# Optimization experiments

Measured on AMD Instinct MI355X. Metric: run time of the kernel, lower is better.

Reference implementation:

```python
import jax, jax.numpy as jnp
import numpy as np

NU = 3
NUM_MEM_TOKENS = 128
EPS = 1e-5


def dpfp(x, nu=NU):
    # x: [..., d] -> [..., 2*nu*d]; all outputs are >= 0
    x = jnp.concatenate([jax.nn.relu(x), jax.nn.relu(-x)], axis=-1)
    x_rolled = jnp.concatenate([jnp.roll(x, shift=j, axis=-1) for j in range(1, nu + 1)], axis=-1)
    x_repeat = jnp.concatenate([x] * nu, axis=-1)
    return x_repeat * x_rolled


def setup_inputs() -> dict:
    key = jax.random.key(0)
    ks = jax.random.split(key, 8)
    B, S, D, DM = 1, 16384, 2048, 64
    DK = 2 * NU * DM  # 384
    scale = 0.02
    return {
        "hidden_states": jax.random.normal(ks[0], (B, S, D), jnp.float32),
        "Wmq": jax.random.normal(ks[1], (DM, D), jnp.float32) * scale,
        "Wmk": jax.random.normal(ks[2], (DM, D), jnp.float32) * scale,
        "Wmv": jax.random.normal(ks[3], (D, D), jnp.float32) * scale,
        "Wmb_w": jax.random.normal(ks[4], (1, D), jnp.float32) * scale,
        "Wmb_b": jax.random.normal(ks[5], (1,), jnp.float32),
        "W_mem": jax.random.normal(ks[6], (B, DK, D), jnp.float32) * scale,
        "z": jax.random.uniform(ks[7], (B, DK), jnp.float32) + 0.1,
    }


def reference(hidden_states, Wmq, Wmk, Wmv, Wmb_w, Wmb_b, W_mem, z):
    # ---- associate (read from fast-weight memory) ----
    mq = dpfp(hidden_states @ Wmq.T)                       # [b,s,dk]
    num = jnp.einsum('ijk,ikt->ijt', mq, W_mem)            # [b,s,d]
    denom = jnp.einsum('ik,ijk->ij', z, mq)[..., None] + EPS
    hidden_states = num / denom + hidden_states

    # wrapped transformer layer modeled as identity
    out = hidden_states

    # ---- update_mem (write: recurrent outer-product accumulation) ----
    mem_tokens = out[:, -NUM_MEM_TOKENS:]                  # [b,m,d]
    mk = dpfp(mem_tokens @ Wmk.T)                          # [b,m,dk]
    new_mv = mem_tokens @ Wmv.T                            # [b,m,d]

    num2 = jnp.einsum('ijk,ikt->ijt', mk, W_mem)           # [b,m,d]
    denom2 = jnp.einsum('ij,ikj->ik', z, mk)[..., None] + EPS
    prev_mv = num2 / denom2

    mk_sq = jnp.sum(mk * mk, axis=-1)                      # ||mk||^2, [b,m]
    new_info_coef = 1.0 - denom2 / (mk_sq + EPS)[..., None]
    new_info_coef = jax.lax.stop_gradient(jnp.clip(new_info_coef, 0.0, 1.0))

    mv = new_mv - prev_mv
    mb = jax.nn.sigmoid(mem_tokens @ Wmb_w.T + Wmb_b)[..., 0]  # [b,m]
    associations = jnp.einsum('ijk,ijt,ij->ikt', mk, mv, mb)   # [b,dk,d]

    W_mem_new = W_mem + associations
    z_new = z + jnp.sum(new_info_coef * mk, axis=1)
    return out, W_mem_new, z_new
```

## Files before the change

kernel.cpp:

```cpp
#include <hip/hip_runtime.h>
#include <hip/hip_bf16.h>
#include <math.h>

#define S_ 16384
#define D_ 2048
#define DM_ 64
#define DK_ 384
#define NMEM_ 128
#define EPS_ 1e-5f

typedef __attribute__((ext_vector_type(8))) short bf16x8;
typedef __attribute__((ext_vector_type(4))) float f32x4;
typedef unsigned short u16;

static __device__ __forceinline__ u16 f2bf(float x) {
    __hip_bfloat16 h = __float2bfloat16(x);
    return *reinterpret_cast<u16*>(&h);
}

static __device__ __forceinline__ void gload16(const void* g, void* l) {
    __builtin_amdgcn_global_load_lds(
        (const __attribute__((address_space(1))) unsigned int*)g,
        (__attribute__((address_space(3))) unsigned int*)l, 16, 0, 0);
}

__global__ __launch_bounds__(256) void k_prep(const float* __restrict__ Wmq,
                                              const float* __restrict__ Wmv,
                                              const float* __restrict__ Wmem,
                                              u16* __restrict__ Wmq_b,
                                              u16* __restrict__ Wmv_b,
                                              u16* __restrict__ WmT) {
    __shared__ float ts[32][33];
    const int bid = blockIdx.x;
    const int tid = threadIdx.x;
    if (bid < 4096) {
        size_t idx = ((size_t)bid * 256 + tid) * 4;
        float4 v = *reinterpret_cast<const float4*>(&Wmv[idx]);
        ushort4 p;
        p.x = f2bf(v.x); p.y = f2bf(v.y); p.z = f2bf(v.z); p.w = f2bf(v.w);
        *reinterpret_cast<ushort4*>(&Wmv_b[idx]) = p;
    } else if (bid < 4224) {
        int idx = ((bid - 4096) * 256 + tid) * 4;
        float4 v = *reinterpret_cast<const float4*>(&Wmq[idx]);
        ushort4 p;
        p.x = f2bf(v.x); p.y = f2bf(v.y); p.z = f2bf(v.z); p.w = f2bf(v.w);
        *reinterpret_cast<ushort4*>(&Wmq_b[idx]) = p;
    } else {
        int t = bid - 4224;
        int c0 = (t & 63) * 32, k0 = (t >> 6) * 32;
        const int tx = tid & 31, ty = tid >> 5;
#pragma unroll
        for (int i = 0; i < 4; ++i)
            ts[ty + 8 * i][tx] = Wmem[(size_t)(k0 + ty + 8 * i) * D_ + c0 + tx];
        __syncthreads();
#pragma unroll
        for (int i = 0; i < 4; ++i)
            WmT[(size_t)(c0 + ty + 8 * i) * DK_ + k0 + tx] = f2bf(ts[tx][ty + 8 * i]);
    }
}

__global__ __launch_bounds__(256) void k_qdp(const float* __restrict__ hs,
                                             const u16* __restrict__ Wmq_b,
                                             const float* __restrict__ z,
                                             u16* __restrict__ mq_b,
                                             float* __restrict__ denomv) {
    __shared__ u16 As[32 * 64];
    __shared__ u16 Bs[64 * 64];
    __shared__ float xs[32][128];
    __shared__ float zs[DK_];
    const int r0 = blockIdx.x * 32;
    const int tid = threadIdx.x;
    const int lane = tid & 63, w = tid >> 6;
    const int lrow = lane & 15, lkg = lane >> 4;
    const int wr = w >> 1, wc = w & 1;
    for (int i = tid; i < DK_; i += 256) zs[i] = z[i];
    f32x4 acc[2];
    const f32x4 zero4 = {0.f, 0.f, 0.f, 0.f};
    acc[0] = zero4; acc[1] = zero4;
    for (int kc = 0; kc < D_ / 64; ++kc) {
#pragma unroll
        for (int i = 0; i < 2; ++i) {
            int flat4 = tid + 256 * i;
            int row = flat4 >> 4, c4 = flat4 & 15;
            const float4 v = *reinterpret_cast<const float4*>(
                &hs[(size_t)(r0 + row) * D_ + kc * 64 + c4 * 4]);
            int off = row * 64 + (((c4 >> 1) ^ (row & 7)) * 8) + (c4 & 1) * 4;
            ushort4 p;
            p.x = f2bf(v.x); p.y = f2bf(v.y); p.z = f2bf(v.z); p.w = f2bf(v.w);
            *reinterpret_cast<ushort4*>(&As[off]) = p;
        }
#pragma unroll
        for (int i = 0; i < 2; ++i) {
            int col = w * 16 + i * 8 + (lane >> 3);
            int gg = (lane & 7) ^ (col & 7);
            gload16(Wmq_b + (size_t)col * D_ + kc * 64 + gg * 8,
                    &Bs[(w * 16 + i * 8) * 64]);
        }
        __syncthreads();
#pragma unroll
        for (int s = 0; s < 2; ++s) {
            int rl = wr * 16 + lrow;
            bf16x8 a_ = *reinterpret_cast<const bf16x8*>(
                &As[rl * 64 + (((s * 4 + lkg) ^ (rl & 7)) * 8)]);
#pragma unroll
            for (int n = 0; n < 2; ++n) {
                int cl = wc * 32 + n * 16 + lrow;
                bf16x8 b_ = *reinterpret_cast<const bf16x8*>(
                    &Bs[cl * 64 + (((s * 4 + lkg) ^ (cl & 7)) * 8)]);
                acc[n] = __builtin_amdgcn_mfma_f32_16x16x32_bf16(a_, b_, acc[n], 0, 0, 0);
            }
        }
        __syncthreads();
    }
#pragma unroll
    for (int n = 0; n < 2; ++n) {
        int col = wc * 32 + n * 16 + lrow;
#pragma unroll
        for (int r = 0; r < 4; ++r) {
            int row = wr * 16 + lkg * 4 + r;
            float q = acc[n][r];
            xs[row][col] = fmaxf(q, 0.f);
            xs[row][col + 64] = fmaxf(-q, 0.f);
        }
    }
    __syncthreads();
    {
        int row = tid >> 3, sub = tid & 7;
        float pd = 0.f;
#pragma unroll
        for (int t = 0; t < 48; ++t) {
            int m = sub * 48 + t;
            int g = m >> 7, i = m & 127;
            float v = xs[row][i] * xs[row][(i - g - 1) & 127];
            mq_b[(size_t)(r0 + row) * DK_ + m] = f2bf(v);
            pd += zs[m] * v;
        }
        pd += __shfl_down(pd, 4, 8);
        pd += __shfl_down(pd, 2, 8);
        pd += __shfl_down(pd, 1, 8);
        if (sub == 0) denomv[r0 + row] = pd + EPS_;
    }
}

__global__ __launch_bounds__(256) void k_main(const float* __restrict__ hs,
                                              const u16* __restrict__ mq_b,
                                              const u16* __restrict__ WmT,
                                              const float* __restrict__ denomv,
                                              float* __restrict__ out) {
    __shared__ u16 At[128 * 128];
    __shared__ u16 Bt[128 * 128];
    __shared__ float dinv[128];
    const int bid = blockIdx.x;
    const int swz = (bid & 7) * 256 + (bid >> 3);
    const int r0 = (swz >> 4) * 128, c0 = (swz & 15) * 128;
    const int tid = threadIdx.x;
    const int lane = tid & 63, w = tid >> 6;
    const int lrow = lane & 15, lkg = lane >> 4;
    const int wr = w >> 1, wc = w & 1;
    if (tid < 128) dinv[tid] = 1.f / denomv[r0 + tid];
    f32x4 acc[4][4];
    const f32x4 zero4 = {0.f, 0.f, 0.f, 0.f};
#pragma unroll
    for (int m = 0; m < 4; ++m)
#pragma unroll
        for (int n = 0; n < 4; ++n) acc[m][n] = zero4;
    for (int kc = 0; kc < 3; ++kc) {
#pragma unroll
        for (int i = 0; i < 8; ++i) {
            int rr = w * 32 + i * 4 + (lane >> 4);
            int gg = (lane & 15) ^ (rr & 7);
            gload16(mq_b + (size_t)(r0 + rr) * DK_ + kc * 128 + gg * 8,
                    &At[(w * 32 + i * 4) * 128]);
            gload16(WmT + (size_t)(c0 + rr) * DK_ + kc * 128 + gg * 8,
                    &Bt[(w * 32 + i * 4) * 128]);
        }
        __syncthreads();
#pragma unroll
        for (int s = 0; s < 4; ++s) {
            bf16x8 af[4], bb[4];
#pragma unroll
            for (int m = 0; m < 4; ++m) {
                int rl = wr * 64 + m * 16 + lrow;
                af[m] = *reinterpret_cast<const bf16x8*>(
                    &At[rl * 128 + (((s * 4 + lkg) ^ (rl & 7)) * 8)]);
            }
#pragma unroll
            for (int n = 0; n < 4; ++n) {
                int cl = wc * 64 + n * 16 + lrow;
                bb[n] = *reinterpret_cast<const bf16x8*>(
                    &Bt[cl * 128 + (((s * 4 + lkg) ^ (cl & 7)) * 8)]);
            }
#pragma unroll
            for (int m = 0; m < 4; ++m)
#pragma unroll
                for (int n = 0; n < 4; ++n)
                    acc[m][n] = __builtin_amdgcn_mfma_f32_16x16x32_bf16(
                        af[m], bb[n], acc[m][n], 0, 0, 0);
        }
        __syncthreads();
    }
#pragma unroll
    for (int m = 0; m < 4; ++m)
#pragma unroll
        for (int n = 0; n < 4; ++n) {
            int colg = c0 + wc * 64 + n * 16 + lrow;
#pragma unroll
            for (int r = 0; r < 4; ++r) {
                int rowl = wr * 64 + m * 16 + lkg * 4 + r;
                size_t off = (size_t)(r0 + rowl) * D_ + colg;
                out[off] = acc[m][n][r] * dinv[rowl] + hs[off];
            }
        }
}

__global__ __launch_bounds__(256) void k_mk(const float* __restrict__ out,
                                            const float* __restrict__ Wmk,
                                            const float* __restrict__ Wmb_w,
                                            const float* __restrict__ Wmb_b,
                                            const float* __restrict__ z,
                                            float* __restrict__ mk_g,
                                            u16* __restrict__ mk_b,
                                            u16* __restrict__ mem_b,
                                            float* __restrict__ scal) {
    __shared__ float memRow[D_];
    __shared__ float qpart[4][64];
    __shared__ float xv[128];
    __shared__ float mks[DK_];
    __shared__ float red[256];
    const int j = blockIdx.x;
    const int tid = threadIdx.x;
    const float* mem = out + (size_t)(S_ - NMEM_ + j) * D_;
    for (int i = tid; i < D_; i += 256) {
        float v = mem[i];
        memRow[i] = v;
        mem_b[(size_t)j * D_ + i] = f2bf(v);
    }
    __syncthreads();
    {
        int c = tid & 63, seg = tid >> 6;
        float p = 0.f;
        for (int k = seg * 512; k < seg * 512 + 512; ++k)
            p += memRow[k] * Wmk[(size_t)c * D_ + k];
        qpart[seg][c] = p;
    }
    __syncthreads();
    if (tid < 64) {
        float q = qpart[0][tid] + qpart[1][tid] + qpart[2][tid] + qpart[3][tid];
        xv[tid] = fmaxf(q, 0.f);
        xv[tid + 64] = fmaxf(-q, 0.f);
    }
    __syncthreads();
    for (int m = tid; m < DK_; m += 256) {
        int i = m & 127, g = m >> 7;
        float v = xv[i] * xv[(i - g - 1) & 127];
        mks[m] = v;
        mk_g[(size_t)j * DK_ + m] = v;
        mk_b[(size_t)j * DK_ + m] = f2bf(v);
    }
    __syncthreads();
    float pd = 0.f, ps = 0.f;
    for (int m = tid; m < DK_; m += 256) { float v = mks[m]; pd += v * z[m]; ps += v * v; }
    red[tid] = pd; __syncthreads();
    for (int s = 128; s > 0; s >>= 1) { if (tid < s) red[tid] += red[tid + s]; __syncthreads(); }
    float denom2 = red[0] + EPS_;
    __syncthreads();
    red[tid] = ps; __syncthreads();
    for (int s = 128; s > 0; s >>= 1) { if (tid < s) red[tid] += red[tid + s]; __syncthreads(); }
    float mksq = red[0];
    __syncthreads();
    float pb = 0.f;
    for (int k = tid; k < D_; k += 256) pb += memRow[k] * Wmb_w[k];
    red[tid] = pb; __syncthreads();
    for (int s = 128; s > 0; s >>= 1) { if (tid < s) red[tid] += red[tid + s]; __syncthreads(); }
    if (tid == 0) {
        float bsum = red[0] + Wmb_b[0];
        float mb = 1.f / (1.f + expf(-bsum));
        float nic = 1.f - denom2 / (mksq + EPS_);
        nic = fminf(fmaxf(nic, 0.f), 1.f);
        scal[j * 4 + 0] = denom2;
        scal[j * 4 + 1] = nic;
        scal[j * 4 + 2] = mb;
        scal[j * 4 + 3] = mksq;
    }
}

__global__ __launch_bounds__(256) void k_mv(const u16* __restrict__ mem_b,
                                            const u16* __restrict__ Wmv_b,
                                            const u16* __restrict__ mk_b,
                                            const u16* __restrict__ WmT,
                                            const float* __restrict__ scal,
                                            float* __restrict__ mvb) {
    __shared__ u16 At[128 * 64];
    __shared__ u16 Bt[64 * 64];
    __shared__ float inv2[128];
    __shared__ float mbl[128];
    const int c0 = blockIdx.x * 64;
    const int tid = threadIdx.x;
    const int lane = tid & 63, w = tid >> 6;
    const int lrow = lane & 15, lkg = lane >> 4;
    const int wr = w >> 1, wc = w & 1;
    if (tid < 128) {
        inv2[tid] = 1.f / scal[tid * 4 + 0];
        mbl[tid] = scal[tid * 4 + 2];
    }
    f32x4 acc1[4][2], acc2[4][2];
    const f32x4 zero4 = {0.f, 0.f, 0.f, 0.f};
#pragma unroll
    for (int m = 0; m < 4; ++m)
#pragma unroll
        for (int n = 0; n < 2; ++n) { acc1[m][n] = zero4; acc2[m][n] = zero4; }
    for (int kc = 0; kc < D_ / 64; ++kc) {
#pragma unroll
        for (int i = 0; i < 4; ++i) {
            int rr = w * 32 + i * 8 + (lane >> 3);
            int gg = (lane & 7) ^ (rr & 7);
            gload16(mem_b + (size_t)rr * D_ + kc * 64 + gg * 8,
                    &At[(w * 32 + i * 8) * 64]);
        }
#pragma unroll
        for (int i = 0; i < 2; ++i) {
            int cc = w * 16 + i * 8 + (lane >> 3);
            int gg = (lane & 7) ^ (cc & 7);
            gload16(Wmv_b + (size_t)(c0 + cc) * D_ + kc * 64 + gg * 8,
                    &Bt[(w * 16 + i * 8) * 64]);
        }
        __syncthreads();
#pragma unroll
        for (int s = 0; s < 2; ++s) {
            bf16x8 af[4], bb[2];
#pragma unroll
            for (int m = 0; m < 4; ++m) {
                int rl = wr * 64 + m * 16 + lrow;
                af[m] = *reinterpret_cast<const bf16x8*>(
                    &At[rl * 64 + (((s * 4 + lkg) ^ (rl & 7)) * 8)]);
            }
#pragma unroll
            for (int n = 0; n < 2; ++n) {
                int cl = wc * 32 + n * 16 + lrow;
                bb[n] = *reinterpret_cast<const bf16x8*>(
                    &Bt[cl * 64 + (((s * 4 + lkg) ^ (cl & 7)) * 8)]);
            }
#pragma unroll
            for (int m = 0; m < 4; ++m)
#pragma unroll
                for (int n = 0; n < 2; ++n)
                    acc1[m][n] = __builtin_amdgcn_mfma_f32_16x16x32_bf16(
                        af[m], bb[n], acc1[m][n], 0, 0, 0);
        }
        __syncthreads();
    }
    for (int kc = 0; kc < 6; ++kc) {
#pragma unroll
        for (int i = 0; i < 4; ++i) {
            int rr = w * 32 + i * 8 + (lane >> 3);
            int gg = (lane & 7) ^ (rr & 7);
            gload16(mk_b + (size_t)rr * DK_ + kc * 64 + gg * 8,
                    &At[(w * 32 + i * 8) * 64]);
        }
#pragma unroll
        for (int i = 0; i < 2; ++i) {
            int cc = w * 16 + i * 8 + (lane >> 3);
            int gg = (lane & 7) ^ (cc & 7);
            gload16(WmT + (size_t)(c0 + cc) * DK_ + kc * 64 + gg * 8,
                    &Bt[(w * 16 + i * 8) * 64]);
        }
        __syncthreads();
#pragma unroll
        for (int s = 0; s < 2; ++s) {
            bf16x8 af[4], bb[2];
#pragma unroll
            for (int m = 0; m < 4; ++m) {
                int rl = wr * 64 + m * 16 + lrow;
                af[m] = *reinterpret_cast<const bf16x8*>(
                    &At[rl * 64 + (((s * 4 + lkg) ^ (rl & 7)) * 8)]);
            }
#pragma unroll
            for (int n = 0; n < 2; ++n) {
                int cl = wc * 32 + n * 16 + lrow;
                bb[n] = *reinterpret_cast<const bf16x8*>(
                    &Bt[cl * 64 + (((s * 4 + lkg) ^ (cl & 7)) * 8)]);
            }
#pragma unroll
            for (int m = 0; m < 4; ++m)
#pragma unroll
                for (int n = 0; n < 2; ++n)
                    acc2[m][n] = __builtin_amdgcn_mfma_f32_16x16x32_bf16(
                        af[m], bb[n], acc2[m][n], 0, 0, 0);
        }
        __syncthreads();
    }
#pragma unroll
    for (int m = 0; m < 4; ++m)
#pragma unroll
        for (int n = 0; n < 2; ++n) {
            int colg = c0 + wc * 32 + n * 16 + lrow;
#pragma unroll
            for (int r = 0; r < 4; ++r) {
                int j = wr * 64 + m * 16 + lkg * 4 + r;
                mvb[(size_t)j * D_ + colg] =
                    (acc1[m][n][r] - acc2[m][n][r] * inv2[j]) * mbl[j];
            }
        }
}

__global__ __launch_bounds__(256) void k_wmem(const float* __restrict__ Wmem,
                                              const float* __restrict__ mk_g,
                                              const float* __restrict__ mvb,
                                              const float* __restrict__ scal,
                                              const float* __restrict__ z,
                                              float* __restrict__ wout,
                                              float* __restrict__ zout) {
    const int tid = threadIdx.x;
    if (blockIdx.y == 48) {
        if (blockIdx.x == 0) {
            for (int t = tid; t < DK_; t += 256) {
                float acc = z[t];
                for (int j = 0; j < NMEM_; ++j)
                    acc += scal[j * 4 + 1] * mk_g[(size_t)j * DK_ + t];
                zout[t] = acc;
            }
        }
        return;
    }
    const int c0 = blockIdx.x * 256;
    const int k0 = blockIdx.y * 8;
    const int tk = tid >> 5, tt = tid & 31;
    float acc[8] = {};
    for (int j = 0; j < NMEM_; ++j) {
        float a = mk_g[(size_t)j * DK_ + k0 + tk];
#pragma unroll
        for (int i = 0; i < 8; ++i)
            acc[i] += a * mvb[(size_t)j * D_ + c0 + tt + 32 * i];
    }
#pragma unroll
    for (int i = 0; i < 8; ++i) {
        size_t off = (size_t)(k0 + tk) * D_ + c0 + tt + 32 * i;
        wout[off] = Wmem[off] + acc[i];
    }
}

extern "C" void kernel_launch(void* const* d_in, const int* in_sizes, int n_in,
                              void* d_out, int out_size, void* d_ws, size_t ws_size,
                              hipStream_t stream) {
    const float* hs   = (const float*)d_in[0];
    const float* Wmq  = (const float*)d_in[1];
    const float* Wmk  = (const float*)d_in[2];
    const float* Wmv  = (const float*)d_in[3];
    const float* Wmbw = (const float*)d_in[4];
    const float* Wmbb = (const float*)d_in[5];
    const float* Wmem = (const float*)d_in[6];
    const float* z    = (const float*)d_in[7];
    float* out  = (float*)d_out;
    float* wout = out + (size_t)S_ * D_;
    float* zout = wout + (size_t)DK_ * D_;

    float* ws = (float*)d_ws;
    float* denomv = ws;
    float* mk_g   = denomv + S_;
    float* scal   = mk_g + (size_t)NMEM_ * DK_;
    float* mvb    = scal + NMEM_ * 4;
    u16* mq_b  = (u16*)(mvb + (size_t)NMEM_ * D_);
    u16* WmT   = mq_b + (size_t)S_ * DK_;
    u16* Wmq_b = WmT + (size_t)D_ * DK_;
    u16* Wmv_b = Wmq_b + (size_t)DM_ * D_;
    u16* mem_b = Wmv_b + (size_t)D_ * D_;
    u16* mk_b  = mem_b + (size_t)NMEM_ * D_;

    k_prep<<<dim3(4992), 256, 0, stream>>>(Wmq, Wmv, Wmem, Wmq_b, Wmv_b, WmT);
    k_qdp<<<dim3(S_ / 32), 256, 0, stream>>>(hs, Wmq_b, z, mq_b, denomv);
    k_main<<<dim3((S_ / 128) * (D_ / 128)), 256, 0, stream>>>(hs, mq_b, WmT, denomv, out);
    k_mk<<<dim3(NMEM_), 256, 0, stream>>>(out, Wmk, Wmbw, Wmbb, z, mk_g, mk_b, mem_b, scal);
    k_mv<<<dim3(D_ / 64), 256, 0, stream>>>(mem_b, Wmv_b, mk_b, WmT, scal, mvb);
    k_wmem<<<dim3(D_ / 256, DK_ / 8 + 1), 256, 0, stream>>>(Wmem, mk_g, mvb, scal, z, wout, zout);
}
```

Before: 206.8 us.

## Fuse prep and query-projection kernels, retile main K-loop, vectorize small kernels

Merges the weight-conversion kernel and the query projection/DPFP kernel into one launch. The query path now reads fp32 Wmq directly and converts it in-kernel with a 128-wide K step, and writes mq with 16-byte stores. The main GEMM uses 64-wide K chunks with smaller LDS tiles, which may allow higher occupancy at the cost of more barriers. k_mk and k_wmem get float4-vectorized loads and stores. The fused kernel's shared-memory footprint is the union of both paths, which can lower occupancy for the Wmv-conversion blocks, and every query block re-converts Wmq.

```diff
diff --git a/kernel.cpp b/kernel.cpp
--- a/kernel.cpp
+++ b/kernel.cpp
@@ -10,6 +10,7 @@
 #define EPS_ 1e-5f
 
 typedef __attribute__((ext_vector_type(8))) short bf16x8;
+typedef __attribute__((ext_vector_type(8))) short s16x8;
 typedef __attribute__((ext_vector_type(4))) float f32x4;
 typedef unsigned short u16;
 
@@ -24,13 +25,20 @@
         (__attribute__((address_space(3))) unsigned int*)l, 16, 0, 0);
 }
 
-__global__ __launch_bounds__(256) void k_prep(const float* __restrict__ Wmq,
-                                              const float* __restrict__ Wmv,
-                                              const float* __restrict__ Wmem,
-                                              u16* __restrict__ Wmq_b,
-                                              u16* __restrict__ Wmv_b,
-                                              u16* __restrict__ WmT) {
+__global__ __launch_bounds__(256) void k_qprep(const float* __restrict__ hs,
+                                               const float* __restrict__ Wmq,
+                                               const float* __restrict__ Wmv,
+                                               const float* __restrict__ Wmem,
+                                               const float* __restrict__ z,
+                                               u16* __restrict__ Wmv_b,
+                                               u16* __restrict__ WmT,
+                                               u16* __restrict__ mq_b,
+                                               float* __restrict__ denomv) {
     __shared__ float ts[32][33];
+    __shared__ u16 As[32 * 128];
+    __shared__ u16 Bs[64 * 128];
+    __shared__ float xs[32][128];
+    __shared__ float zs[DK_];
     const int bid = blockIdx.x;
     const int tid = threadIdx.x;
     if (bid < 4096) {
@@ -39,14 +47,10 @@
         ushort4 p;
         p.x = f2bf(v.x); p.y = f2bf(v.y); p.z = f2bf(v.z); p.w = f2bf(v.w);
         *reinterpret_cast<ushort4*>(&Wmv_b[idx]) = p;
-    } else if (bid < 4224) {
-        int idx = ((bid - 4096) * 256 + tid) * 4;
-        float4 v = *reinterpret_cast<const float4*>(&Wmq[idx]);
-        ushort4 p;
-        p.x = f2bf(v.x); p.y = f2bf(v.y); p.z = f2bf(v.z); p.w = f2bf(v.w);
-        *reinterpret_cast<ushort4*>(&Wmq_b[idx]) = p;
-    } else {
-        int t = bid - 4224;
+        return;
+    }
+    if (bid < 4864) {
+        int t = bid - 4096;
         int c0 = (t & 63) * 32, k0 = (t >> 6) * 32;
         const int tx = tid & 31, ty = tid >> 5;
 #pragma unroll
@@ -56,20 +60,9 @@
 #pragma unroll
         for (int i = 0; i < 4; ++i)
             WmT[(size_t)(c0 + ty + 8 * i) * DK_ + k0 + tx] = f2bf(ts[tx][ty + 8 * i]);
-    }
-}
-
-__global__ __launch_bounds__(256) void k_qdp(const float* __restrict__ hs,
-                                             const u16* __restrict__ Wmq_b,
-                                             const float* __restrict__ z,
-                                             u16* __restrict__ mq_b,
-                                             float* __restrict__ denomv) {
-    __shared__ u16 As[32 * 64];
-    __shared__ u16 Bs[64 * 64];
-    __shared__ float xs[32][128];
-    __shared__ float zs[DK_];
-    const int r0 = blockIdx.x * 32;
-    const int tid = threadIdx.x;
+        return;
+    }
+    const int r0 = (bid - 4864) * 32;
     const int lane = tid & 63, w = tid >> 6;
     const int lrow = lane & 15, lkg = lane >> 4;
     const int wr = w >> 1, wc = w & 1;
@@ -77,36 +70,40 @@
     f32x4 acc[2];
     const f32x4 zero4 = {0.f, 0.f, 0.f, 0.f};
     acc[0] = zero4; acc[1] = zero4;
-    for (int kc = 0; kc < D_ / 64; ++kc) {
-#pragma unroll
-        for (int i = 0; i < 2; ++i) {
+    for (int kc = 0; kc < D_ / 128; ++kc) {
+#pragma unroll
+        for (int i = 0; i < 4; ++i) {
             int flat4 = tid + 256 * i;
-            int row = flat4 >> 4, c4 = flat4 & 15;
+            int row = flat4 >> 5, c4 = flat4 & 31;
             const float4 v = *reinterpret_cast<const float4*>(
-                &hs[(size_t)(r0 + row) * D_ + kc * 64 + c4 * 4]);
-            int off = row * 64 + (((c4 >> 1) ^ (row & 7)) * 8) + (c4 & 1) * 4;
+                &hs[(size_t)(r0 + row) * D_ + kc * 128 + c4 * 4]);
+            int off = row * 128 + (((c4 >> 1) ^ (row & 7)) * 8) + (c4 & 1) * 4;
             ushort4 p;
             p.x = f2bf(v.x); p.y = f2bf(v.y); p.z = f2bf(v.z); p.w = f2bf(v.w);
             *reinterpret_cast<ushort4*>(&As[off]) = p;
         }
 #pragma unroll
-        for (int i = 0; i < 2; ++i) {
-            int col = w * 16 + i * 8 + (lane >> 3);
-            int gg = (lane & 7) ^ (col & 7);
-            gload16(Wmq_b + (size_t)col * D_ + kc * 64 + gg * 8,
-                    &Bs[(w * 16 + i * 8) * 64]);
-        }
-        __syncthreads();
-#pragma unroll
-        for (int s = 0; s < 2; ++s) {
+        for (int i = 0; i < 8; ++i) {
+            int flat4 = tid + 256 * i;
+            int row = flat4 >> 5, c4 = flat4 & 31;
+            const float4 v = *reinterpret_cast<const float4*>(
+                &Wmq[(size_t)row * D_ + kc * 128 + c4 * 4]);
+            int off = row * 128 + (((c4 >> 1) ^ (row & 7)) * 8) + (c4 & 1) * 4;
+            ushort4 p;
+            p.x = f2bf(v.x); p.y = f2bf(v.y); p.z = f2bf(v.z); p.w = f2bf(v.w);
+            *reinterpret_cast<ushort4*>(&Bs[off]) = p;
+        }
+        __syncthreads();
+#pragma unroll
+        for (int s = 0; s < 4; ++s) {
             int rl = wr * 16 + lrow;
             bf16x8 a_ = *reinterpret_cast<const bf16x8*>(
-                &As[rl * 64 + (((s * 4 + lkg) ^ (rl & 7)) * 8)]);
+                &As[rl * 128 + (((s * 4 + lkg) ^ (rl & 7)) * 8)]);
 #pragma unroll
             for (int n = 0; n < 2; ++n) {
                 int cl = wc * 32 + n * 16 + lrow;
                 bf16x8 b_ = *reinterpret_cast<const bf16x8*>(
-                    &Bs[cl * 64 + (((s * 4 + lkg) ^ (cl & 7)) * 8)]);
+                    &Bs[cl * 128 + (((s * 4 + lkg) ^ (cl & 7)) * 8)]);
                 acc[n] = __builtin_amdgcn_mfma_f32_16x16x32_bf16(a_, b_, acc[n], 0, 0, 0);
             }
         }
@@ -128,12 +125,19 @@
         int row = tid >> 3, sub = tid & 7;
         float pd = 0.f;
 #pragma unroll
-        for (int t = 0; t < 48; ++t) {
-            int m = sub * 48 + t;
-            int g = m >> 7, i = m & 127;
-            float v = xs[row][i] * xs[row][(i - g - 1) & 127];
-            mq_b[(size_t)(r0 + row) * DK_ + m] = f2bf(v);
-            pd += zs[m] * v;
+        for (int c = 0; c < 6; ++c) {
+            int base = sub * 48 + c * 8;
+            int g = base >> 7;
+            s16x8 pk;
+#pragma unroll
+            for (int e = 0; e < 8; ++e) {
+                int m = base + e;
+                int i = m & 127;
+                float v = xs[row][i] * xs[row][(i - g - 1) & 127];
+                pd += zs[m] * v;
+                pk[e] = (short)f2bf(v);
+            }
+            *reinterpret_cast<s16x8*>(&mq_b[(size_t)(r0 + row) * DK_ + base]) = pk;
         }
         pd += __shfl_down(pd, 4, 8);
         pd += __shfl_down(pd, 2, 8);
@@ -147,8 +151,8 @@
                                               const u16* __restrict__ WmT,
                                               const float* __restrict__ denomv,
                                               float* __restrict__ out) {
-    __shared__ u16 At[128 * 128];
-    __shared__ u16 Bt[128 * 128];
+    __shared__ u16 At[128 * 64];
+    __shared__ u16 Bt[128 * 64];
     __shared__ float dinv[128];
     const int bid = blockIdx.x;
     const int swz = (bid & 7) * 256 + (bid >> 3);
@@ -164,31 +168,31 @@
     for (int m = 0; m < 4; ++m)
 #pragma unroll
         for (int n = 0; n < 4; ++n) acc[m][n] = zero4;
-    for (int kc = 0; kc < 3; ++kc) {
-#pragma unroll
-        for (int i = 0; i < 8; ++i) {
-            int rr = w * 32 + i * 4 + (lane >> 4);
-            int gg = (lane & 15) ^ (rr & 7);
-            gload16(mq_b + (size_t)(r0 + rr) * DK_ + kc * 128 + gg * 8,
-                    &At[(w * 32 + i * 4) * 128]);
-            gload16(WmT + (size_t)(c0 + rr) * DK_ + kc * 128 + gg * 8,
-                    &Bt[(w * 32 + i * 4) * 128]);
-        }
-        __syncthreads();
-#pragma unroll
-        for (int s = 0; s < 4; ++s) {
+    for (int kc = 0; kc < 6; ++kc) {
+#pragma unroll
+        for (int i = 0; i < 4; ++i) {
+            int rr = w * 32 + i * 8 + (lane >> 3);
+            int gg = (lane & 7) ^ (rr & 7);
+            gload16(mq_b + (size_t)(r0 + rr) * DK_ + kc * 64 + gg * 8,
+                    &At[(w * 32 + i * 8) * 64]);
+            gload16(WmT + (size_t)(c0 + rr) * DK_ + kc * 64 + gg * 8,
+                    &Bt[(w * 32 + i * 8) * 64]);
+        }
+        __syncthreads();
+#pragma unroll
+        for (int s = 0; s < 2; ++s) {
             bf16x8 af[4], bb[4];
 #pragma unroll
             for (int m = 0; m < 4; ++m) {
                 int rl = wr * 64 + m * 16 + lrow;
                 af[m] = *reinterpret_cast<const bf16x8*>(
-                    &At[rl * 128 + (((s * 4 + lkg) ^ (rl & 7)) * 8)]);
+                    &At[rl * 64 + (((s * 4 + lkg) ^ (rl & 7)) * 8)]);
             }
 #pragma unroll
             for (int n = 0; n < 4; ++n) {
                 int cl = wc * 64 + n * 16 + lrow;
                 bb[n] = *reinterpret_cast<const bf16x8*>(
-                    &Bt[cl * 128 + (((s * 4 + lkg) ^ (cl & 7)) * 8)]);
+                    &Bt[cl * 64 + (((s * 4 + lkg) ^ (cl & 7)) * 8)]);
             }
 #pragma unroll
             for (int m = 0; m < 4; ++m)
@@ -230,17 +234,26 @@
     const int j = blockIdx.x;
     const int tid = threadIdx.x;
     const float* mem = out + (size_t)(S_ - NMEM_ + j) * D_;
-    for (int i = tid; i < D_; i += 256) {
-        float v = mem[i];
-        memRow[i] = v;
-        mem_b[(size_t)j * D_ + i] = f2bf(v);
+    const float4* mem4 = reinterpret_cast<const float4*>(mem);
+    float4* mr4 = reinterpret_cast<float4*>(memRow);
+#pragma unroll
+    for (int i4 = tid; i4 < 512; i4 += 256) {
+        float4 v = mem4[i4];
+        mr4[i4] = v;
+        ushort4 p;
+        p.x = f2bf(v.x); p.y = f2bf(v.y); p.z = f2bf(v.z); p.w = f2bf(v.w);
+        *reinterpret_cast<ushort4*>(&mem_b[(size_t)j * D_ + i4 * 4]) = p;
     }
     __syncthreads();
     {
         int c = tid & 63, seg = tid >> 6;
+        const float4* wrow = reinterpret_cast<const float4*>(Wmk + (size_t)c * D_);
         float p = 0.f;
-        for (int k = seg * 512; k < seg * 512 + 512; ++k)
-            p += memRow[k] * Wmk[(size_t)c * D_ + k];
+#pragma unroll 4
+        for (int k4 = seg * 128; k4 < seg * 128 + 128; ++k4) {
+            float4 a = mr4[k4], b = wrow[k4];
+            p += a.x * b.x + a.y * b.y + a.z * b.z + a.w * b.w;
+        }
         qpart[seg][c] = p;
     }
     __syncthreads();
@@ -269,7 +282,14 @@
     float mksq = red[0];
     __syncthreads();
     float pb = 0.f;
-    for (int k = tid; k < D_; k += 256) pb += memRow[k] * Wmb_w[k];
+    {
+        const float4* wb4 = reinterpret_cast<const float4*>(Wmb_w);
+#pragma unroll
+        for (int k4 = tid; k4 < 512; k4 += 256) {
+            float4 a = mr4[k4], b = wb4[k4];
+            pb += a.x * b.x + a.y * b.y + a.z * b.z + a.w * b.w;
+        }
+    }
     red[tid] = pb; __syncthreads();
     for (int s = 128; s > 0; s >>= 1) { if (tid < s) red[tid] += red[tid + s]; __syncthreads(); }
     if (tid == 0) {
@@ -425,17 +445,26 @@
     const int c0 = blockIdx.x * 256;
     const int k0 = blockIdx.y * 8;
     const int tk = tid >> 5, tt = tid & 31;
-    float acc[8] = {};
+    const float4* mvb4 = reinterpret_cast<const float4*>(mvb);
+    f32x4 acc[2] = {{0.f, 0.f, 0.f, 0.f}, {0.f, 0.f, 0.f, 0.f}};
+#pragma unroll 4
     for (int j = 0; j < NMEM_; ++j) {
         float a = mk_g[(size_t)j * DK_ + k0 + tk];
 #pragma unroll
-        for (int i = 0; i < 8; ++i)
-            acc[i] += a * mvb[(size_t)j * D_ + c0 + tt + 32 * i];
-    }
-#pragma unroll
-    for (int i = 0; i < 8; ++i) {
-        size_t off = (size_t)(k0 + tk) * D_ + c0 + tt + 32 * i;
-        wout[off] = Wmem[off] + acc[i];
+        for (int i = 0; i < 2; ++i) {
+            float4 v = mvb4[((size_t)j * D_ + c0 + tt * 4 + 128 * i) >> 2];
+            acc[i][0] += a * v.x; acc[i][1] += a * v.y;
+            acc[i][2] += a * v.z; acc[i][3] += a * v.w;
+        }
+    }
+#pragma unroll
+    for (int i = 0; i < 2; ++i) {
+        size_t off = (size_t)(k0 + tk) * D_ + c0 + tt * 4 + 128 * i;
+        float4 wv = *reinterpret_cast<const float4*>(&Wmem[off]);
+        float4 o;
+        o.x = wv.x + acc[i][0]; o.y = wv.y + acc[i][1];
+        o.z = wv.z + acc[i][2]; o.w = wv.w + acc[i][3];
+        *reinterpret_cast<float4*>(&wout[off]) = o;
     }
 }
 
@@ -461,13 +490,12 @@
     float* mvb    = scal + NMEM_ * 4;
     u16* mq_b  = (u16*)(mvb + (size_t)NMEM_ * D_);
     u16* WmT   = mq_b + (size_t)S_ * DK_;
-    u16* Wmq_b = WmT + (size_t)D_ * DK_;
-    u16* Wmv_b = Wmq_b + (size_t)DM_ * D_;
+    u16* Wmv_b = WmT + (size_t)D_ * DK_;
     u16* mem_b = Wmv_b + (size_t)D_ * D_;
     u16* mk_b  = mem_b + (size_t)NMEM_ * D_;
 
-    k_prep<<<dim3(4992), 256, 0, stream>>>(Wmq, Wmv, Wmem, Wmq_b, Wmv_b, WmT);
-    k_qdp<<<dim3(S_ / 32), 256, 0, stream>>>(hs, Wmq_b, z, mq_b, denomv);
+    k_qprep<<<dim3(4864 + S_ / 32), 256, 0, stream>>>(hs, Wmq, Wmv, Wmem, z,
+                                                      Wmv_b, WmT, mq_b, denomv);
     k_main<<<dim3((S_ / 128) * (D_ / 128)), 256, 0, stream>>>(hs, mq_b, WmT, denomv, out);
     k_mk<<<dim3(NMEM_), 256, 0, stream>>>(out, Wmk, Wmbw, Wmbb, z, mk_g, mk_b, mem_b, scal);
     k_mv<<<dim3(D_ / 64), 256, 0, stream>>>(mem_b, Wmv_b, mk_b, WmT, scal, mvb);
```

Result: no change. 209.0 us (+1.1%).
